# Optimization experiments

Hardware: AMD Instinct MI355X
Metric: run time of the kernel (lower is better)

Reference implementation:

```python
import jax, jax.numpy as jnp
import numpy as np

B, N, D = 4, 2048, 1024
H, HD = 16, 64
MAX_SEQ = 4096
INNER = H * HD


def setup_inputs() -> dict:
    key = jax.random.key(0)
    ks = jax.random.split(key, 5)
    s = 0.02
    return {
        "x": jax.random.normal(ks[0], (B, N, D), dtype=jnp.float32),
        "ln_gamma": jnp.ones((D,), jnp.float32),
        "ln_beta": jnp.zeros((D,), jnp.float32),
        "w_qkv": jax.random.normal(ks[1], (D, 3 * INNER), dtype=jnp.float32) * s,
        "w_out": jax.random.normal(ks[2], (INNER, D), dtype=jnp.float32) * s,
        "b_out": jnp.zeros((D,), jnp.float32),
    }


def _rope_tables(n, head_dim):
    inv_freq = 1.0 / (10000.0 ** (jnp.arange(0, head_dim, 2, dtype=jnp.float32) / head_dim))
    pos = jnp.arange(n, dtype=jnp.float32)
    ang = pos[:, None] * inv_freq[None, :]  # [n, hd/2]
    return jnp.sin(ang), jnp.cos(ang)


def reference(x, ln_gamma, ln_beta, w_qkv, w_out, b_out):
    b, n, d = x.shape
    # LayerNorm
    mu = jnp.mean(x, axis=-1, keepdims=True)
    var = jnp.var(x, axis=-1, keepdims=True)
    xn = (x - mu) / jnp.sqrt(var + 1e-5) * ln_gamma + ln_beta
    # QKV projection (no bias)
    qkv = xn @ w_qkv  # [b, n, 3*inner]
    q, k, v = jnp.split(qkv, 3, axis=-1)
    def to_heads(t):
        return t.reshape(b, n, H, HD).transpose(0, 2, 1, 3)  # b h n d
    q, k, v = to_heads(q), to_heads(k), to_heads(v)
    # RoPE (half-split rotation, as in source)
    sin, cos = _rope_tables(n, HD)  # [n, hd/2]
    sin = sin[None, None]
    cos = cos[None, None]
    half = HD // 2
    def rotate(t):
        t1, t2 = t[..., :half], t[..., half:]
        return jnp.concatenate([t1 * cos - t2 * sin, t2 * cos + t1 * sin], axis=-1)
    qr, kr = rotate(q), rotate(k)
    scale = HD ** -0.5
    scores = jnp.einsum('bhid,bhjd->bhij', qr, kr) * scale
    probs = jax.nn.softmax(scores, axis=-1)
    out = jnp.einsum('bhij,bhjd->bhid', probs, v)
    out = out.transpose(0, 2, 1, 3).reshape(b, n, INNER)
    return out @ w_out + b_out
```

## Files before the change

kernel.cpp:

```cpp
#include <hip/hip_runtime.h>
#include <hip/hip_bf16.h>

#define Bb   4
#define Nn   2048
#define Dd   1024
#define Hh   16
#define HDd  64
#define IN3  3072
#define RR   8192

typedef __attribute__((ext_vector_type(8))) short short8;
typedef __attribute__((ext_vector_type(4))) float floatx4;

#define MFMA16(a, b, c) __builtin_amdgcn_mfma_f32_16x16x32_bf16((a), (b), (c), 0, 0, 0)

static __device__ __forceinline__ unsigned short f2bf(float f) {
    union { float f; unsigned int u; } v; v.f = f;
    unsigned int r = v.u + 0x7fffu + ((v.u >> 16) & 1u);
    return (unsigned short)(r >> 16);
}
static __device__ __forceinline__ float bf2f(unsigned short h) {
    union { unsigned int u; float f; } v; v.u = ((unsigned int)h) << 16;
    return v.f;
}

static __device__ __forceinline__ float fast_exp2(float x) {
#if __has_builtin(__builtin_amdgcn_exp2f)
    return __builtin_amdgcn_exp2f(x);
#else
    return exp2f(x);
#endif
}

static __device__ __forceinline__ void sincos_rev(float ang, float& s, float& c) {
#if __has_builtin(__builtin_amdgcn_sinf) && __has_builtin(__builtin_amdgcn_cosf)
    float rev = ang * 0.15915494309189535f;
    rev = rev - floorf(rev);
    s = __builtin_amdgcn_sinf(rev);
    c = __builtin_amdgcn_cosf(rev);
#else
    s = sinf(ang);
    c = cosf(ang);
#endif
}

typedef const __attribute__((address_space(1))) void* gas1_t;
typedef __attribute__((address_space(3))) void* las3_t;
static __device__ __forceinline__ void load_lds16(const void* g, void* l) {
    __builtin_amdgcn_global_load_lds((gas1_t)(unsigned long long)g,
                                     (las3_t)(unsigned int)(unsigned long long)l,
                                     16, 0, 0);
}

__global__ void transpose_w(const float* __restrict__ src, unsigned short* __restrict__ dst,
                            int rows, int cols) {
    __shared__ float tile[32][33];
    int c0 = blockIdx.x * 32, r0 = blockIdx.y * 32;
    int tx = threadIdx.x, ty = threadIdx.y;
#pragma unroll
    for (int i = 0; i < 4; ++i) tile[ty + 8 * i][tx] = src[(r0 + ty + 8 * i) * cols + c0 + tx];
    __syncthreads();
#pragma unroll
    for (int i = 0; i < 4; ++i) dst[(c0 + ty + 8 * i) * rows + r0 + tx] = f2bf(tile[tx][ty + 8 * i]);
}

__global__ __launch_bounds__(256) void ln_kernel(const float* __restrict__ x,
                                                 const float* __restrict__ g,
                                                 const float* __restrict__ be,
                                                 unsigned short* __restrict__ xn) {
    int row = blockIdx.x, t = threadIdx.x;
    float4 v = ((const float4*)(x + row * Dd))[t];
    float s  = v.x + v.y + v.z + v.w;
    float sq = v.x * v.x + v.y * v.y + v.z * v.z + v.w * v.w;
#pragma unroll
    for (int off = 1; off < 64; off <<= 1) { s += __shfl_xor(s, off); sq += __shfl_xor(sq, off); }
    __shared__ float ps[4], pq2[4];
    int wv = t >> 6;
    if ((t & 63) == 0) { ps[wv] = s; pq2[wv] = sq; }
    __syncthreads();
    s  = ps[0] + ps[1] + ps[2] + ps[3];
    sq = pq2[0] + pq2[1] + pq2[2] + pq2[3];
    float mu   = s * (1.0f / Dd);
    float var  = sq * (1.0f / Dd) - mu * mu;
    float rstd = rsqrtf(var + 1e-5f);
    float4 gg = ((const float4*)g)[t];
    float4 bb = ((const float4*)be)[t];
    ushort4 o;
    o.x = f2bf((v.x - mu) * rstd * gg.x + bb.x);
    o.y = f2bf((v.y - mu) * rstd * gg.y + bb.y);
    o.z = f2bf((v.z - mu) * rstd * gg.z + bb.z);
    o.w = f2bf((v.w - mu) * rstd * gg.w + bb.w);
    ((ushort4*)(xn + row * Dd))[t] = o;
}

__global__ __launch_bounds__(256) void gemm_qkv(const unsigned short* __restrict__ A,
                                                const unsigned short* __restrict__ Bt,
                                                unsigned short* __restrict__ qo,
                                                unsigned short* __restrict__ ko,
                                                unsigned short* __restrict__ vo) {
    __shared__ unsigned short As[128 * 64];
    __shared__ unsigned short Bs[128 * 64];
    int r0 = blockIdx.x * 128, c0 = blockIdx.y * 128;
    int tid = threadIdx.x;
    int wave = tid >> 6, lane = tid & 63, l15 = lane & 15, quad = lane >> 4;
    int wm = wave & 1, wn = wave >> 1;
    floatx4 acc[4][4] = {};
    int swz0 = (quad ^ (l15 & 7)) << 3;
    int swz1 = ((4 | quad) ^ (l15 & 7)) << 3;
    for (int k0 = 0; k0 < 1024; k0 += 64) {
#pragma unroll
        for (int i = 0; i < 4; ++i) {
            int c = wave * 4 + i;
            int p = c * 64 + lane;
            int row = p >> 3, pr = p & 7;
            int sc = pr ^ (row & 7);
            load_lds16(&A[(r0 + row) * 1024 + k0 + sc * 8],  &As[p * 8]);
            load_lds16(&Bt[(c0 + row) * 1024 + k0 + sc * 8], &Bs[p * 8]);
        }
        __syncthreads();
#pragma unroll
        for (int ks = 0; ks < 2; ++ks) {
            int sw = ks ? swz1 : swz0;
            short8 af[4], bf[4];
#pragma unroll
            for (int mi = 0; mi < 4; ++mi)
                af[mi] = *(const short8*)&As[(wm * 64 + mi * 16 + l15) * 64 + sw];
#pragma unroll
            for (int ni = 0; ni < 4; ++ni)
                bf[ni] = *(const short8*)&Bs[(wn * 64 + ni * 16 + l15) * 64 + sw];
#pragma unroll
            for (int mi = 0; mi < 4; ++mi)
#pragma unroll
                for (int ni = 0; ni < 4; ++ni)
                    acc[mi][ni] = MFMA16(af[mi], bf[ni], acc[mi][ni]);
        }
        __syncthreads();
    }
    if (c0 < 2048) {
        const float crope = 13.287712379549449f / 32.0f;
        float invf0 = fast_exp2(-(float)l15 * crope);
        float invf1 = fast_exp2(-(float)(l15 + 16) * crope);
#pragma unroll
        for (int mi = 0; mi < 4; ++mi)
#pragma unroll
            for (int r2 = 0; r2 < 4; ++r2) {
                int rr = r0 + wm * 64 + mi * 16 + quad * 4 + r2;
                float n = (float)(rr & 2047);
                float s0, c0r, s1, c1r;
                sincos_rev(n * invf0, s0, c0r);
                sincos_rev(n * invf1, s1, c1r);
                float t1a = acc[mi][0][r2], t2a = acc[mi][2][r2];
                acc[mi][0][r2] = t1a * c0r - t2a * s0;
                acc[mi][2][r2] = t2a * c0r + t1a * s0;
                float t1b = acc[mi][1][r2], t2b = acc[mi][3][r2];
                acc[mi][1][r2] = t1b * c1r - t2b * s1;
                acc[mi][3][r2] = t2b * c1r + t1b * s1;
            }
    }
    unsigned short* outp = (c0 < 1024) ? qo : (c0 < 2048) ? ko : vo;
#pragma unroll
    for (int ni = 0; ni < 4; ++ni) {
        int c = c0 + wn * 64 + ni * 16 + l15;
        int cin = c & 1023;
        int h = cin >> 6, j = cin & 63;
#pragma unroll
        for (int mi = 0; mi < 4; ++mi) {
#pragma unroll
            for (int r2 = 0; r2 < 4; ++r2) {
                int rr = r0 + wm * 64 + mi * 16 + quad * 4 + r2;
                int b = rr >> 11, n = rr & 2047;
                int bh = b * 16 + h;
                outp[(bh * 2048 + n) * 64 + j] = f2bf(acc[mi][ni][r2]);
            }
        }
    }
}

__global__ __launch_bounds__(256) void vtrans(const unsigned short* __restrict__ v,
                                              unsigned short* __restrict__ vt) {
    __shared__ unsigned short T[64][72];
    int bh = blockIdx.y, n0 = blockIdx.x * 64;
    int t = threadIdx.x;
    int nl = t >> 2, c = (t & 3) * 16;
    const unsigned short* src = v + ((bh * 2048) + n0 + nl) * 64 + c;
    *(short8*)&T[nl][c]     = *(const short8*)src;
    *(short8*)&T[nl][c + 8] = *(const short8*)(src + 8);
    __syncthreads();
    int hd = t >> 2, nc = (t & 3) * 16;
    unsigned short tmp[16];
#pragma unroll
    for (int i = 0; i < 16; ++i) {
        int pos = nc + i;
        int blk = pos >> 5, p = pos & 31;
        int kq = (p >> 3) & 3, hh = (p >> 2) & 1, r = p & 3;
        tmp[i] = T[blk * 32 + hh * 16 + kq * 4 + r][hd];
    }
    unsigned short* dst = vt + ((bh * 64) + hd) * 2048 + n0 + nc;
    *(short8*)dst       = *(const short8*)&tmp[0];
    *(short8*)(dst + 8) = *(const short8*)&tmp[8];
}

__global__ __launch_bounds__(256, 2) void attn_kernel(const unsigned short* __restrict__ q,
                                                      const unsigned short* __restrict__ k,
                                                      const unsigned short* __restrict__ vt,
                                                      unsigned short* __restrict__ attn) {
    __shared__ unsigned short KVs[2][2][64 * 64];
    int bh = blockIdx.y, q0 = blockIdx.x * 256;
    int tid = threadIdx.x;
    int wave = tid >> 6, lane = tid & 63, l15 = lane & 15, quad = lane >> 4;
    const unsigned short* qb  = q  + bh * (Nn * HDd);
    const unsigned short* kbp = k  + bh * (Nn * HDd);
    const unsigned short* vb  = vt + bh * (HDd * Nn);
    int qbase = q0 + wave * 64;

    short8 bq[4][2];
#pragma unroll
    for (int g = 0; g < 4; ++g) {
        bq[g][0] = *(const short8*)&qb[(qbase + g * 16 + l15) * 64 + quad * 8];
        bq[g][1] = *(const short8*)&qb[(qbase + g * 16 + l15) * 64 + 32 + quad * 8];
    }

    auto stage = [&](int buf, int kb0) {
#pragma unroll
        for (int i = 0; i < 2; ++i) {
            int c = wave * 2 + i;
            int p = c * 64 + lane;
            int row = p >> 3, pr = p & 7;
            int sc = pr ^ (row & 7);
            load_lds16(&kbp[(kb0 + row) * 64 + sc * 8], &KVs[buf][0][p * 8]);
            load_lds16(&vb[row * Nn + kb0 + sc * 8],    &KVs[buf][1][p * 8]);
        }
    };

    floatx4 ot[4][4] = {};
    float l_run[4] = {0.0f, 0.0f, 0.0f, 0.0f};
    const float sc2 = 0.125f * 1.4426950408889634f;
    int swz0 = (quad ^ (l15 & 7)) << 3;
    int swz1 = ((4 | quad) ^ (l15 & 7)) << 3;

    auto body = [&](int cur, int kt) {
        if (kt < 31) stage(cur ^ 1, (kt + 1) * 64);
        const unsigned short* Kc = KVs[cur][0];
        const unsigned short* Vc = KVs[cur][1];
        short8 ka0[4], ka1[4];
#pragma unroll
        for (int mb = 0; mb < 4; ++mb) {
            ka0[mb] = *(const short8*)&Kc[(mb * 16 + l15) * 64 + swz0];
            ka1[mb] = *(const short8*)&Kc[(mb * 16 + l15) * 64 + swz1];
        }
        short8 bv0[4], bv1[4];
#pragma unroll
        for (int ht = 0; ht < 4; ++ht) {
            int row = (ht * 16 + l15) * 64;
            bv0[ht] = *(const short8*)&Vc[row + swz0];
            bv1[ht] = *(const short8*)&Vc[row + swz1];
        }
#pragma unroll
        for (int g = 0; g < 4; ++g) {
            floatx4 st[4];
#pragma unroll
            for (int mb = 0; mb < 4; ++mb) {
                floatx4 z = {0.0f, 0.0f, 0.0f, 0.0f};
                z = MFMA16(ka0[mb], bq[g][0], z);
                st[mb] = MFMA16(ka1[mb], bq[g][1], z);
            }
            short8 pa[2];
            float sump = 0.0f;
#pragma unroll
            for (int c = 0; c < 2; ++c) {
                union { ushort4 u[2]; short8 s; } w;
#pragma unroll
                for (int t2 = 0; t2 < 2; ++t2) {
                    int mb = 2 * c + t2;
                    float p0 = fast_exp2(st[mb][0] * sc2);
                    float p1 = fast_exp2(st[mb][1] * sc2);
                    float p2 = fast_exp2(st[mb][2] * sc2);
                    float p3 = fast_exp2(st[mb][3] * sc2);
                    sump += (p0 + p1) + (p2 + p3);
                    *(__hip_bfloat162*)&w.u[t2].x = __float22bfloat162_rn(float2{p0, p1});
                    *(__hip_bfloat162*)&w.u[t2].z = __float22bfloat162_rn(float2{p2, p3});
                }
                pa[c] = w.s;
            }
            l_run[g] += sump;
#pragma unroll
            for (int ht = 0; ht < 4; ++ht) {
                ot[g][ht] = MFMA16(pa[0], bv0[ht], ot[g][ht]);
                ot[g][ht] = MFMA16(pa[1], bv1[ht], ot[g][ht]);
            }
        }
        __syncthreads();
    };

    stage(0, 0);
    __syncthreads();
    for (int kt = 0; kt < 32; kt += 2) {
        body(0, kt);
        body(1, kt + 1);
    }
    int b = bh >> 4, h = bh & 15;
    unsigned short* ob = ((unsigned short*)KVs) + wave * 1152;
#pragma unroll
    for (int g = 0; g < 4; ++g) {
        float l = l_run[g];
        l += __shfl_xor(l, 16);
        l += __shfl_xor(l, 32);
        float invl = 1.0f / l;
        float il[4];
#pragma unroll
        for (int r = 0; r < 4; ++r) il[r] = __shfl(invl, quad * 4 + r);
#pragma unroll
        for (int ht = 0; ht < 4; ++ht)
#pragma unroll
            for (int r = 0; r < 4; ++r)
                ob[(quad * 4 + r) * 72 + ht * 16 + l15] = f2bf(ot[g][ht][r] * il[r]);
        int q_loc = lane >> 2, seg = lane & 3;
        unsigned short* dst = attn + ((long)(b * Nn + q0 + wave * 64 + g * 16 + q_loc)) * 1024 + h * 64 + seg * 16;
        *(short8*)dst       = *(const short8*)&ob[q_loc * 72 + seg * 16];
        *(short8*)(dst + 8) = *(const short8*)&ob[q_loc * 72 + seg * 16 + 8];
    }
}

__global__ __launch_bounds__(256) void gemm_out(const unsigned short* __restrict__ A,
                                                const unsigned short* __restrict__ Bt,
                                                const float* __restrict__ bout,
                                                float* __restrict__ out) {
    __shared__ unsigned short As[128 * 64];
    __shared__ unsigned short Bs[128 * 64];
    int r0 = blockIdx.x * 128, c0 = blockIdx.y * 128;
    int tid = threadIdx.x;
    int wave = tid >> 6, lane = tid & 63, l15 = lane & 15, quad = lane >> 4;
    int wm = wave & 1, wn = wave >> 1;
    floatx4 acc[4][4] = {};
    int swz0 = (quad ^ (l15 & 7)) << 3;
    int swz1 = ((4 | quad) ^ (l15 & 7)) << 3;
    for (int k0 = 0; k0 < 1024; k0 += 64) {
#pragma unroll
        for (int i = 0; i < 4; ++i) {
            int c = wave * 4 + i;
            int p = c * 64 + lane;
            int row = p >> 3, pr = p & 7;
            int sc = pr ^ (row & 7);
            load_lds16(&A[(r0 + row) * 1024 + k0 + sc * 8],  &As[p * 8]);
            load_lds16(&Bt[(c0 + row) * 1024 + k0 + sc * 8], &Bs[p * 8]);
        }
        __syncthreads();
#pragma unroll
        for (int ks = 0; ks < 2; ++ks) {
            int sw = ks ? swz1 : swz0;
            short8 af[4], bf[4];
#pragma unroll
            for (int mi = 0; mi < 4; ++mi)
                af[mi] = *(const short8*)&As[(wm * 64 + mi * 16 + l15) * 64 + sw];
#pragma unroll
            for (int ni = 0; ni < 4; ++ni)
                bf[ni] = *(const short8*)&Bs[(wn * 64 + ni * 16 + l15) * 64 + sw];
#pragma unroll
            for (int mi = 0; mi < 4; ++mi)
#pragma unroll
                for (int ni = 0; ni < 4; ++ni)
                    acc[mi][ni] = MFMA16(af[mi], bf[ni], acc[mi][ni]);
        }
        __syncthreads();
    }
#pragma unroll
    for (int ni = 0; ni < 4; ++ni) {
        int c = c0 + wn * 64 + ni * 16 + l15;
        float bias = bout[c];
#pragma unroll
        for (int mi = 0; mi < 4; ++mi)
#pragma unroll
            for (int r2 = 0; r2 < 4; ++r2) {
                int rr = r0 + wm * 64 + mi * 16 + quad * 4 + r2;
                out[rr * 1024 + c] = acc[mi][ni][r2] + bias;
            }
    }
}

extern "C" void kernel_launch(void* const* d_in, const int* in_sizes, int n_in,
                              void* d_out, int out_size, void* d_ws, size_t ws_size,
                              hipStream_t stream) {
    const float* x    = (const float*)d_in[0];
    const float* g    = (const float*)d_in[1];
    const float* be   = (const float*)d_in[2];
    const float* wqkv = (const float*)d_in[3];
    const float* wout = (const float*)d_in[4];
    const float* bout = (const float*)d_in[5];
    float* out = (float*)d_out;

    char* ws = (char*)d_ws;
    unsigned short* xn    = (unsigned short*)(ws);
    unsigned short* wqkvT = (unsigned short*)(ws + 16777216);
    unsigned short* woutT = (unsigned short*)(ws + 23068672);
    unsigned short* qb    = (unsigned short*)(ws + 25165824);
    unsigned short* kb    = (unsigned short*)(ws + 41943040);
    unsigned short* vt    = (unsigned short*)(ws + 58720256);
    unsigned short* attn  = (unsigned short*)(ws + 75497472);
    unsigned short* vtmp  = attn;

    transpose_w<<<dim3(IN3 / 32, Dd / 32), dim3(32, 8), 0, stream>>>(wqkv, wqkvT, Dd, IN3);
    transpose_w<<<dim3(Dd / 32, Dd / 32), dim3(32, 8), 0, stream>>>(wout, woutT, Dd, Dd);
    ln_kernel<<<RR, 256, 0, stream>>>(x, g, be, xn);
    gemm_qkv<<<dim3(RR / 128, IN3 / 128), 256, 0, stream>>>(xn, wqkvT, qb, kb, vtmp);
    vtrans<<<dim3(Nn / 64, Bb * Hh), 256, 0, stream>>>(vtmp, vt);
    attn_kernel<<<dim3(Nn / 256, Bb * Hh), 256, 0, stream>>>(qb, kb, vt, attn);
    gemm_out<<<dim3(RR / 128, Dd / 128), 256, 0, stream>>>(attn, woutT, bout, out);
}
```

Baseline: 275.5 us.

## Enlarge QKV GEMM tile to 256x256 with double-buffered, interleaved LDS prefetch

The QKV projection GEMM moves from a 128x128 tile with 4 waves to a 256x256 tile with 8 waves, using a double-buffered LDS layout. Global-to-LDS loads for the next k-step are issued in pieces between four MFMA sub-phases, with explicit vmcnt/lgkmcnt waits, barriers and s_setprio. The aim is to hide load latency and improve operand reuse per byte loaded. The trade-offs are a 128KB LDS footprint that allows only one block per CU, and fewer blocks (384) spread unevenly over the CUs.

```diff
diff --git a/kernel.cpp b/kernel.cpp
--- a/kernel.cpp
+++ b/kernel.cpp
@@ -93,58 +93,143 @@
     ((ushort4*)(xn + row * Dd))[t] = o;
 }
 
-__global__ __launch_bounds__(256) void gemm_qkv(const unsigned short* __restrict__ A,
-                                                const unsigned short* __restrict__ Bt,
-                                                unsigned short* __restrict__ qo,
-                                                unsigned short* __restrict__ ko,
-                                                unsigned short* __restrict__ vo) {
-    __shared__ unsigned short As[128 * 64];
-    __shared__ unsigned short Bs[128 * 64];
-    int r0 = blockIdx.x * 128, c0 = blockIdx.y * 128;
+__global__ __launch_bounds__(512, 2) void gemm_qkv(const unsigned short* __restrict__ A,
+                                                   const unsigned short* __restrict__ Bt,
+                                                   unsigned short* __restrict__ qo,
+                                                   unsigned short* __restrict__ ko,
+                                                   unsigned short* __restrict__ vo) {
+    __shared__ unsigned short LDS[65536];
+    int r0 = blockIdx.x * 256, c0 = blockIdx.y * 256;
     int tid = threadIdx.x;
-    int wave = tid >> 6, lane = tid & 63, l15 = lane & 15, quad = lane >> 4;
-    int wm = wave & 1, wn = wave >> 1;
-    floatx4 acc[4][4] = {};
+    int wv = tid >> 6, lane = tid & 63, l15 = lane & 15, quad = lane >> 4;
+    int wm = wv >> 2, wn = wv & 3;
+
+    floatx4 acc[8][4] = {};
     int swz0 = (quad ^ (l15 & 7)) << 3;
     int swz1 = ((4 | quad) ^ (l15 & 7)) << 3;
-    for (int k0 = 0; k0 < 1024; k0 += 64) {
-#pragma unroll
-        for (int i = 0; i < 4; ++i) {
-            int c = wave * 4 + i;
-            int p = c * 64 + lane;
-            int row = p >> 3, pr = p & 7;
-            int sc = pr ^ (row & 7);
-            load_lds16(&A[(r0 + row) * 1024 + k0 + sc * 8],  &As[p * 8]);
-            load_lds16(&Bt[(c0 + row) * 1024 + k0 + sc * 8], &Bs[p * 8]);
-        }
-        __syncthreads();
-#pragma unroll
-        for (int ks = 0; ks < 2; ++ks) {
-            int sw = ks ? swz1 : swz0;
-            short8 af[4], bf[4];
-#pragma unroll
-            for (int mi = 0; mi < 4; ++mi)
-                af[mi] = *(const short8*)&As[(wm * 64 + mi * 16 + l15) * 64 + sw];
-#pragma unroll
-            for (int ni = 0; ni < 4; ++ni)
-                bf[ni] = *(const short8*)&Bs[(wn * 64 + ni * 16 + l15) * 64 + sw];
-#pragma unroll
-            for (int mi = 0; mi < 4; ++mi)
-#pragma unroll
-                for (int ni = 0; ni < 4; ++ni)
-                    acc[mi][ni] = MFMA16(af[mi], bf[ni], acc[mi][ni]);
-        }
-        __syncthreads();
-    }
+    const int abase = wm * 8192 + l15 * 64;
+    const int bbase = 16384 + (wn >> 1) * 8192 + ((wn & 1) * 64 + l15) * 64;
+
+    auto stageA = [&](int tt, int half) {
+        unsigned short* base = &LDS[(tt & 1) * 32768 + half * 8192];
+        int k0 = tt * 64;
+#pragma unroll
+        for (int i = 0; i < 2; ++i) {
+            int q = (wv * 2 + i) * 64 + lane;
+            int row = q >> 3, cp = q & 7;
+            int sc = cp ^ (row & 7);
+            load_lds16(&A[(r0 + half * 128 + row) * 1024 + k0 + sc * 8], &base[q * 8]);
+        }
+    };
+    auto stageB = [&](int tt, int half) {
+        unsigned short* base = &LDS[(tt & 1) * 32768 + 16384 + half * 8192];
+        int k0 = tt * 64;
+#pragma unroll
+        for (int i = 0; i < 2; ++i) {
+            int q = (wv * 2 + i) * 64 + lane;
+            int row = q >> 3, cp = q & 7;
+            int sc = cp ^ (row & 7);
+            load_lds16(&Bt[(c0 + half * 128 + row) * 1024 + k0 + sc * 8], &base[q * 8]);
+        }
+    };
+
+    stageA(0, 0); stageA(0, 1); stageB(0, 0); stageB(0, 1);
+    stageA(1, 0); stageA(1, 1);
+    asm volatile("s_waitcnt vmcnt(4)" ::: "memory");
+    __builtin_amdgcn_s_barrier();
+
+    for (int t = 0; t < 16; ++t) {
+        int bufo = (t & 1) * 32768;
+        short8 a0[4][2], a1[4][2], b0[2][2], b1[2][2];
+
+        if (t < 15) stageB(t + 1, 0);
+#pragma unroll
+        for (int mi = 0; mi < 4; ++mi) {
+            a0[mi][0] = *(const short8*)&LDS[bufo + abase + (mi * 16) * 64 + swz0];
+            a0[mi][1] = *(const short8*)&LDS[bufo + abase + (mi * 16) * 64 + swz1];
+        }
+#pragma unroll
+        for (int ni = 0; ni < 2; ++ni) {
+            b0[ni][0] = *(const short8*)&LDS[bufo + bbase + (ni * 16) * 64 + swz0];
+            b0[ni][1] = *(const short8*)&LDS[bufo + bbase + (ni * 16) * 64 + swz1];
+        }
+        __builtin_amdgcn_s_barrier();
+        asm volatile("s_waitcnt lgkmcnt(0)" ::: "memory");
+        __builtin_amdgcn_s_setprio(1);
+#pragma unroll
+        for (int ks = 0; ks < 2; ++ks)
+#pragma unroll
+            for (int mi = 0; mi < 4; ++mi)
+#pragma unroll
+                for (int ni = 0; ni < 2; ++ni)
+                    acc[mi][ni] = MFMA16(a0[mi][ks], b0[ni][ks], acc[mi][ni]);
+        __builtin_amdgcn_s_setprio(0);
+        __builtin_amdgcn_s_barrier();
+
+        if (t < 15) stageB(t + 1, 1);
+#pragma unroll
+        for (int mi = 0; mi < 4; ++mi) {
+            a1[mi][0] = *(const short8*)&LDS[bufo + abase + ((64 + mi * 16)) * 64 + swz0];
+            a1[mi][1] = *(const short8*)&LDS[bufo + abase + ((64 + mi * 16)) * 64 + swz1];
+        }
+        __builtin_amdgcn_s_barrier();
+        asm volatile("s_waitcnt lgkmcnt(0)" ::: "memory");
+        __builtin_amdgcn_s_setprio(1);
+#pragma unroll
+        for (int ks = 0; ks < 2; ++ks)
+#pragma unroll
+            for (int mi = 0; mi < 4; ++mi)
+#pragma unroll
+                for (int ni = 0; ni < 2; ++ni)
+                    acc[4 + mi][ni] = MFMA16(a1[mi][ks], b0[ni][ks], acc[4 + mi][ni]);
+        __builtin_amdgcn_s_setprio(0);
+        __builtin_amdgcn_s_barrier();
+
+        if (t < 14) stageA(t + 2, 0);
+#pragma unroll
+        for (int ni = 0; ni < 2; ++ni) {
+            b1[ni][0] = *(const short8*)&LDS[bufo + bbase + ((32 + ni * 16)) * 64 + swz0];
+            b1[ni][1] = *(const short8*)&LDS[bufo + bbase + ((32 + ni * 16)) * 64 + swz1];
+        }
+        __builtin_amdgcn_s_barrier();
+        asm volatile("s_waitcnt lgkmcnt(0)" ::: "memory");
+        __builtin_amdgcn_s_setprio(1);
+#pragma unroll
+        for (int ks = 0; ks < 2; ++ks)
+#pragma unroll
+            for (int mi = 0; mi < 4; ++mi)
+#pragma unroll
+                for (int ni = 0; ni < 2; ++ni)
+                    acc[4 + mi][2 + ni] = MFMA16(a1[mi][ks], b1[ni][ks], acc[4 + mi][2 + ni]);
+        __builtin_amdgcn_s_setprio(0);
+        __builtin_amdgcn_s_barrier();
+
+        if (t < 14) stageA(t + 2, 1);
+        __builtin_amdgcn_s_barrier();
+        asm volatile("s_waitcnt lgkmcnt(0)" ::: "memory");
+        __builtin_amdgcn_s_setprio(1);
+#pragma unroll
+        for (int ks = 0; ks < 2; ++ks)
+#pragma unroll
+            for (int mi = 0; mi < 4; ++mi)
+#pragma unroll
+                for (int ni = 0; ni < 2; ++ni)
+                    acc[mi][2 + ni] = MFMA16(a0[mi][ks], b1[ni][ks], acc[mi][2 + ni]);
+        __builtin_amdgcn_s_setprio(0);
+        if (t < 14)       asm volatile("s_waitcnt vmcnt(4)" ::: "memory");
+        else if (t == 14) asm volatile("s_waitcnt vmcnt(0)" ::: "memory");
+        __builtin_amdgcn_s_barrier();
+    }
+
     if (c0 < 2048) {
         const float crope = 13.287712379549449f / 32.0f;
         float invf0 = fast_exp2(-(float)l15 * crope);
         float invf1 = fast_exp2(-(float)(l15 + 16) * crope);
 #pragma unroll
-        for (int mi = 0; mi < 4; ++mi)
+        for (int mi = 0; mi < 8; ++mi)
 #pragma unroll
             for (int r2 = 0; r2 < 4; ++r2) {
-                int rr = r0 + wm * 64 + mi * 16 + quad * 4 + r2;
+                int rr = r0 + wm * 128 + mi * 16 + quad * 4 + r2;
                 float n = (float)(rr & 2047);
                 float s0, c0r, s1, c1r;
                 sincos_rev(n * invf0, s0, c0r);
@@ -164,10 +249,10 @@
         int cin = c & 1023;
         int h = cin >> 6, j = cin & 63;
 #pragma unroll
-        for (int mi = 0; mi < 4; ++mi) {
+        for (int mi = 0; mi < 8; ++mi) {
 #pragma unroll
             for (int r2 = 0; r2 < 4; ++r2) {
-                int rr = r0 + wm * 64 + mi * 16 + quad * 4 + r2;
+                int rr = r0 + wm * 128 + mi * 16 + quad * 4 + r2;
                 int b = rr >> 11, n = rr & 2047;
                 int bh = b * 16 + h;
                 outp[(bh * 2048 + n) * 64 + j] = f2bf(acc[mi][ni][r2]);
@@ -401,7 +486,7 @@
     transpose_w<<<dim3(IN3 / 32, Dd / 32), dim3(32, 8), 0, stream>>>(wqkv, wqkvT, Dd, IN3);
     transpose_w<<<dim3(Dd / 32, Dd / 32), dim3(32, 8), 0, stream>>>(wout, woutT, Dd, Dd);
     ln_kernel<<<RR, 256, 0, stream>>>(x, g, be, xn);
-    gemm_qkv<<<dim3(RR / 128, IN3 / 128), 256, 0, stream>>>(xn, wqkvT, qb, kb, vtmp);
+    gemm_qkv<<<dim3(RR / 256, IN3 / 256), 512, 0, stream>>>(xn, wqkvT, qb, kb, vtmp);
     vtrans<<<dim3(Nn / 64, Bb * Hh), 256, 0, stream>>>(vtmp, vt);
     attn_kernel<<<dim3(Nn / 256, Bb * Hh), 256, 0, stream>>>(qb, kb, vt, attn);
     gemm_out<<<dim3(RR / 128, Dd / 128), 256, 0, stream>>>(attn, woutT, bout, out);
```

Result: no change. 271.6 us (-1.4%).
